# Performance work log

Measured on AMD Instinct MI355X. Metric: run time of the kernel, lower is better.

## Reference

```python
import jax, jax.numpy as jnp
import numpy as np

D_MODEL = 1024
K_QUERY = 32
K_TOPK = 4

def setup_inputs() -> dict:
    key = jax.random.key(0)
    k1, k2, k3, k4, k5 = jax.random.split(key, 5)
    x = jax.random.normal(k1, (4, 2048, D_MODEL), dtype=jnp.float32)
    # nn.Linear(d_model, k_query): weight [k_query, d_model], bias [k_query]
    sc = 1.0 / np.sqrt(D_MODEL)
    Wq = jax.random.uniform(k2, (K_QUERY, D_MODEL), jnp.float32, -sc, sc)
    bq = jax.random.uniform(k3, (K_QUERY,), jnp.float32, -sc, sc)
    Wk = jax.random.uniform(k4, (K_QUERY, D_MODEL), jnp.float32, -sc, sc)
    bk = jax.random.uniform(k5, (K_QUERY,), jnp.float32, -sc, sc)
    return {"x": x, "Wq": Wq, "bq": bq, "Wk": Wk, "bk": bk}

def reference(x, Wq, bq, Wk, bk):
    # x: [B, T, D]
    queries = jnp.einsum('btd,kd->btk', x, Wq) + bq      # [B, T, Kq]
    keys = jnp.einsum('btd,kd->btk', x, Wk) + bk         # [B, T, Kq]
    sim = jnp.einsum('btk,bsk->bts', queries, keys)      # [B, T, T]
    sim = sim / jnp.sqrt(jnp.float32(queries.shape[-1]))
    _, topk_idx = jax.lax.top_k(sim, K_TOPK)              # [B, T, K]
    # gather neighbors per (b, t): x[b, topk_idx[b, t]] -> [B, T, K, D]
    neighbors = jax.vmap(lambda xb, ib: xb[ib])(x, topk_idx)
    gathered = neighbors.mean(axis=2)                     # [B, T, D]
    return gathered
```

## Files before the change

kernel.cpp:

```cpp
#include <hip/hip_runtime.h>
#include <math.h>

#define D_MODEL 1024
#define T_SEQ   2048
#define NBATCH  4
#define NROWS   (NBATCH * T_SEQ)
#define NOUT    64

#define T16F   1024

typedef float  v4f  __attribute__((ext_vector_type(4)));
typedef _Float16 v8hf __attribute__((ext_vector_type(8)));

__device__ __forceinline__ bool key_gt(float av, int ai, float bv, int bi) {
    return (av > bv) || (av == bv && ai < bi);
}

__device__ __forceinline__ void cmpswap(float& v0, int& i0, float& v1, int& i1) {
    bool sw = key_gt(v1, i1, v0, i0);
    float nv0 = sw ? v1 : v0, nv1 = sw ? v0 : v1;
    int   ni0 = sw ? i1 : i0, ni1 = sw ? i0 : i1;
    v0 = nv0; v1 = nv1; i0 = ni0; i1 = ni1;
}

__device__ __forceinline__ void merge4(float (&a)[4], int (&ai)[4],
                                       float b0, int j0, float b1, int j1,
                                       float b2, int j2, float b3, int j3) {
    if (!key_gt(a[0], ai[0], b3, j3)) { a[0] = b3; ai[0] = j3; }
    if (!key_gt(a[1], ai[1], b2, j2)) { a[1] = b2; ai[1] = j2; }
    if (!key_gt(a[2], ai[2], b1, j1)) { a[2] = b1; ai[2] = j1; }
    if (!key_gt(a[3], ai[3], b0, j0)) { a[3] = b0; ai[3] = j0; }
    cmpswap(a[0], ai[0], a[2], ai[2]);
    cmpswap(a[1], ai[1], a[3], ai[3]);
    cmpswap(a[0], ai[0], a[1], ai[1]);
    cmpswap(a[2], ai[2], a[3], ai[3]);
}

__device__ __forceinline__ void insert4(float (&tv)[4], int (&tix)[4], float v, int idx) {
    if (v > tv[3]) {
        bool g0 = v > tv[0], g1 = v > tv[1], g2 = v > tv[2];
        float n0 = g0 ? v : tv[0];
        int   m0 = g0 ? idx : tix[0];
        float n1 = g1 ? (g0 ? tv[0] : v) : tv[1];
        int   m1 = g1 ? (g0 ? tix[0] : idx) : tix[1];
        float n2 = g2 ? (g1 ? tv[1] : v) : tv[2];
        int   m2 = g2 ? (g1 ? tix[1] : idx) : tix[2];
        float n3 = g2 ? tv[2] : v;
        int   m3 = g2 ? tix[2] : idx;
        tv[0] = n0; tv[1] = n1; tv[2] = n2; tv[3] = n3;
        tix[0] = m0; tix[1] = m1; tix[2] = m2; tix[3] = m3;
    }
}

__device__ void run_probe16(int tid, int* __restrict__ tab)
{
    __shared__ _Float16 A16[16][32];
    __shared__ _Float16 B16[32][16];
    __shared__ float    D16[16][16];

    for (int e = tid; e < 512; e += 256) {
        const int m = e >> 5, k = e & 31;
        A16[m][k] = (_Float16)(float)(1 + (3 * m + 5 * k) % 61);
        const int kk = e >> 4, n = e & 15;
        B16[kk][n] = (_Float16)(float)(1 + (7 * kk + 11 * n) % 59);
    }
    __syncthreads();
    {
        const int m = tid >> 4, n = tid & 15;
        float s = 0.f;
        for (int k = 0; k < 32; ++k) s += (float)A16[m][k] * (float)B16[k][n];
        D16[m][n] = s;
    }
    __syncthreads();

    if (tid >= 64) return;
    const int lane = tid;

    v8hf a, b;
    const int ab = (lane >> 4) * 8;
    #pragma unroll
    for (int j = 0; j < 8; ++j) {
        a[j] = A16[lane & 15][ab + j];
        b[j] = B16[ab + j][lane & 15];
    }
    v4f c = {0.f, 0.f, 0.f, 0.f};
    c = __builtin_amdgcn_mfma_f32_16x16x32_f16(a, b, c, 0, 0, 0);

    bool ok0 = true;
    #pragma unroll
    for (int i = 0; i < 4; ++i)
        ok0 = ok0 && (c[i] == D16[4 * (lane >> 4) + i][lane & 15]);
    if (lane == 0) tab[T16F] = __all(ok0) ? 0 : -1;
}

__global__ __launch_bounds__(256) void wprep_probe(
    const float* __restrict__ Wq, const float* __restrict__ Wk,
    double* __restrict__ Wdt, _Float16* __restrict__ Wh, _Float16* __restrict__ Wl,
    int* __restrict__ tab)
{
    const int tid = threadIdx.x;
    const int idx = blockIdx.x * 256 + tid;

    {
        const int o = idx & 63;
        const int d = idx >> 6;
        float v = (o < 32) ? Wq[(size_t)o * D_MODEL + d]
                           : Wk[(size_t)(o - 32) * D_MODEL + d];
        Wdt[(size_t)d * 64 + o] = (double)v;
    }
    {
        const int o = idx >> 10;
        const int d = idx & 1023;
        float v = (o < 32) ? Wq[(size_t)o * D_MODEL + d]
                           : Wk[(size_t)(o - 32) * D_MODEL + d];
        _Float16 h = (_Float16)v;
        Wh[(size_t)o * D_MODEL + d] = h;
        Wl[(size_t)o * D_MODEL + d] = (_Float16)(v - (float)h);
    }

    if (blockIdx.x == 0) run_probe16(tid, tab);
}

__global__ __launch_bounds__(512) void proj(
    const float* __restrict__ x, const double* __restrict__ Wdt,
    const _Float16* __restrict__ Wh, const _Float16* __restrict__ Wl,
    const float* __restrict__ bq, const float* __restrict__ bk_,
    const int* __restrict__ tab,
    float* __restrict__ Qt, float* __restrict__ Kt,
    _Float16* __restrict__ Qh, _Float16* __restrict__ Ql,
    _Float16* __restrict__ Kh, _Float16* __restrict__ Kl)
{
    __shared__ float  comb[4][64][4];
    __shared__ double combd[4][64][4];

    const int tid  = threadIdx.x;
    const int lane = tid & 63;
    const int wav  = tid >> 6;
    const int og   = __builtin_amdgcn_readfirstlane(wav >> 1);
    const int half = __builtin_amdgcn_readfirstlane(wav & 1);
    const int row0 = blockIdx.x * 16;
    const int kb   = half * 512;

    if (tab[T16F] == 0) {
        const int m  = lane & 15;
        const int ko = (lane >> 4) * 8;
        const float*    xrow  = x  + (size_t)(row0 + m) * D_MODEL + kb + ko;
        const _Float16* whrow = Wh + (size_t)(og * 16 + m) * D_MODEL + kb + ko;
        const _Float16* wlrow = Wl + (size_t)(og * 16 + m) * D_MODEL + kb + ko;

        v4f hh = {0.f, 0.f, 0.f, 0.f};
        v4f hl = {0.f, 0.f, 0.f, 0.f};
        v4f lh = {0.f, 0.f, 0.f, 0.f};
        #pragma unroll 4
        for (int kc = 0; kc < 16; ++kc) {
            float4 x0 = *reinterpret_cast<const float4*>(xrow + kc * 32);
            float4 x1 = *reinterpret_cast<const float4*>(xrow + kc * 32 + 4);
            const float f[8] = {x0.x, x0.y, x0.z, x0.w, x1.x, x1.y, x1.z, x1.w};
            v8hf ah, al;
            #pragma unroll
            for (int e = 0; e < 8; ++e) {
                _Float16 h = (_Float16)f[e];
                ah[e] = h;
                al[e] = (_Float16)(f[e] - (float)h);
            }
            v8hf bh = *reinterpret_cast<const v8hf*>(whrow + kc * 32);
            v8hf bl = *reinterpret_cast<const v8hf*>(wlrow + kc * 32);
            hh = __builtin_amdgcn_mfma_f32_16x16x32_f16(ah, bh, hh, 0, 0, 0);
            hl = __builtin_amdgcn_mfma_f32_16x16x32_f16(ah, bl, hl, 0, 0, 0);
            lh = __builtin_amdgcn_mfma_f32_16x16x32_f16(al, bh, lh, 0, 0, 0);
        }

        v4f tot;
        #pragma unroll
        for (int i = 0; i < 4; ++i) tot[i] = (hh[i] + hl[i]) + lh[i];

        if (half == 1) {
            #pragma unroll
            for (int i = 0; i < 4; ++i) comb[og][lane][i] = tot[i];
        }
        __syncthreads();
        if (half == 0) {
            #pragma unroll
            for (int i = 0; i < 4; ++i) {
                const float t = tot[i] + comb[og][lane][i];
                const int dmv = 4 * (lane >> 4) + i;
                const int o   = og * 16 + m;
                const int row = row0 + dmv;
                const float bias = (o < 32) ? bq[o] : bk_[o - 32];
                const float v = t + bias;
                const _Float16 h = (_Float16)v;
                const _Float16 l = (_Float16)(v - (float)h);
                if (o < 32) {
                    Qh[(size_t)row * 32 + o] = h;
                    Ql[(size_t)row * 32 + o] = l;
                } else {
                    Kh[(size_t)row * 32 + (o - 32)] = h;
                    Kl[(size_t)row * 32 + (o - 32)] = l;
                }
            }
        }
        return;
    }

    {
        const int n  = lane & 15;
        const int r4 = (lane >> 4) * 4;
        const int o  = og * 16 + n;
        const double* wcol = Wdt + o;
        double acc[4] = {0.0, 0.0, 0.0, 0.0};
        for (int dd = 0; dd < 512; ++dd) {
            const int d = kb + dd;
            double wv = wcol[(size_t)d * 64];
            #pragma unroll
            for (int i = 0; i < 4; ++i)
                acc[i] = fma((double)x[(size_t)(row0 + r4 + i) * D_MODEL + d], wv, acc[i]);
        }
        if (half == 1) {
            #pragma unroll
            for (int i = 0; i < 4; ++i) combd[og][lane][i] = acc[i];
        }
        __syncthreads();
        if (half == 0) {
            #pragma unroll
            for (int i = 0; i < 4; ++i) {
                const double t = acc[i] + combd[og][lane][i];
                const int row = row0 + r4 + i;
                const int bb  = row >> 11, tt = row & 2047;
                const double bias = (o < 32) ? (double)bq[o] : (double)bk_[o - 32];
                const float v = (float)(t + bias);
                if (o < 32) Qt[((size_t)bb * 32 + o) * T_SEQ + tt] = v;
                else        Kt[((size_t)bb * 32 + (o - 32)) * T_SEQ + tt] = v;
            }
        }
    }
}

__global__ __launch_bounds__(512) void sim_topk_gather(
    const float* __restrict__ x,
    const _Float16* __restrict__ Qh, const _Float16* __restrict__ Ql,
    const _Float16* __restrict__ Kh, const _Float16* __restrict__ Kl,
    const float* __restrict__ Qt, const float* __restrict__ Kt,
    const int* __restrict__ tab,
    float* __restrict__ out)
{
    __shared__ float sV[8][16][4];
    __shared__ int   sI[8][16][4];
    __shared__ float sVf[16][32][4];
    __shared__ int   sIf[16][32][4];
    __shared__ int   topIdx[16][4];

    const int tid  = threadIdx.x;
    const int lane = tid & 63;
    const int wav  = tid >> 6;
    const int tt   = blockIdx.x & 127;
    const int b    = blockIdx.x >> 7;
    const int row0g = b * T_SEQ + tt * 16;

    if (tab[T16F] == 0) {
        const int m  = lane & 15;
        const int ko = (lane >> 4) * 8;
        v8hf ah = *reinterpret_cast<const v8hf*>(Qh + (size_t)(row0g + m) * 32 + ko);
        v8hf al = *reinterpret_cast<const v8hf*>(Ql + (size_t)(row0g + m) * 32 + ko);
        const _Float16* KhB = Kh + (size_t)b * T_SEQ * 32;
        const _Float16* KlB = Kl + (size_t)b * T_SEQ * 32;

        float tv[4][4]; int tix[4][4];
        #pragma unroll
        for (int r = 0; r < 4; ++r)
            #pragma unroll
            for (int j = 0; j < 4; ++j) { tv[r][j] = -INFINITY; tix[r][j] = 0x7fffffff; }

        const int sq = wav * 256;
        #pragma unroll 4
        for (int st = 0; st < 16; ++st) {
            const int s0 = sq + st * 16;
            v8hf bh = *reinterpret_cast<const v8hf*>(KhB + (size_t)(s0 + m) * 32 + ko);
            v8hf bl = *reinterpret_cast<const v8hf*>(KlB + (size_t)(s0 + m) * 32 + ko);
            v4f c = {0.f, 0.f, 0.f, 0.f};
            c = __builtin_amdgcn_mfma_f32_16x16x32_f16(ah, bh, c, 0, 0, 0);
            c = __builtin_amdgcn_mfma_f32_16x16x32_f16(ah, bl, c, 0, 0, 0);
            c = __builtin_amdgcn_mfma_f32_16x16x32_f16(al, bh, c, 0, 0, 0);
            c = __builtin_amdgcn_mfma_f32_16x16x32_f16(al, bl, c, 0, 0, 0);
            const int col = s0 + m;
            #pragma unroll
            for (int i = 0; i < 4; ++i) insert4(tv[i], tix[i], c[i], col);
        }

        #pragma unroll
        for (int mk = 1; mk <= 8; mk <<= 1) {
            #pragma unroll
            for (int r = 0; r < 4; ++r) {
                float b0 = __shfl_xor(tv[r][0], mk, 64);
                float b1 = __shfl_xor(tv[r][1], mk, 64);
                float b2 = __shfl_xor(tv[r][2], mk, 64);
                float b3 = __shfl_xor(tv[r][3], mk, 64);
                int   j0 = __shfl_xor(tix[r][0], mk, 64);
                int   j1 = __shfl_xor(tix[r][1], mk, 64);
                int   j2 = __shfl_xor(tix[r][2], mk, 64);
                int   j3 = __shfl_xor(tix[r][3], mk, 64);
                merge4(tv[r], tix[r], b0, j0, b1, j1, b2, j2, b3, j3);
            }
        }

        if ((lane & 15) == 0) {
            const int rbase = (lane >> 4) * 4;
            #pragma unroll
            for (int r = 0; r < 4; ++r)
                #pragma unroll
                for (int j = 0; j < 4; ++j) {
                    sV[wav][rbase + r][j] = tv[r][j];
                    sI[wav][rbase + r][j] = tix[r][j];
                }
        }
        __syncthreads();

        if (tid < 16) {
            float mv[4]; int mi[4];
            #pragma unroll
            for (int j = 0; j < 4; ++j) { mv[j] = sV[0][tid][j]; mi[j] = sI[0][tid][j]; }
            #pragma unroll
            for (int w = 1; w < 8; ++w)
                merge4(mv, mi,
                       sV[w][tid][0], sI[w][tid][0],
                       sV[w][tid][1], sI[w][tid][1],
                       sV[w][tid][2], sI[w][tid][2],
                       sV[w][tid][3], sI[w][tid][3]);
            #pragma unroll
            for (int j = 0; j < 4; ++j) topIdx[tid][j] = mi[j];
        }
        __syncthreads();
    } else {
        const float* QtB = Qt + (size_t)b * 32 * T_SEQ;
        const float* KtB = Kt + (size_t)b * 32 * T_SEQ;
        const int row   = tid >> 5;
        const int chunk = tid & 31;
        const int trow  = tt * 16 + row;
        float q[32];
        #pragma unroll 8
        for (int i = 0; i < 32; ++i) q[i] = QtB[(size_t)i * T_SEQ + trow];
        float tv4[4]; int tix4[4];
        #pragma unroll
        for (int j = 0; j < 4; ++j) { tv4[j] = -INFINITY; tix4[j] = 0x7fffffff; }
        const int sbeg = chunk * 64;
        for (int s = sbeg; s < sbeg + 64; ++s) {
            float sum = 0.f;
            #pragma unroll 8
            for (int i = 0; i < 32; ++i)
                sum = fmaf(q[i], KtB[(size_t)i * T_SEQ + s], sum);
            insert4(tv4, tix4, sum, s);
        }
        #pragma unroll
        for (int j = 0; j < 4; ++j) { sVf[row][chunk][j] = tv4[j]; sIf[row][chunk][j] = tix4[j]; }
        __syncthreads();
        if (tid < 16) {
            float mv[4]; int mi[4];
            #pragma unroll
            for (int j = 0; j < 4; ++j) { mv[j] = sVf[tid][0][j]; mi[j] = sIf[tid][0][j]; }
            for (int cc = 1; cc < 32; ++cc)
                merge4(mv, mi,
                       sVf[tid][cc][0], sIf[tid][cc][0],
                       sVf[tid][cc][1], sIf[tid][cc][1],
                       sVf[tid][cc][2], sIf[tid][cc][2],
                       sVf[tid][cc][3], sIf[tid][cc][3]);
            #pragma unroll
            for (int j = 0; j < 4; ++j) topIdx[tid][j] = mi[j];
        }
        __syncthreads();
    }

    const float* xb = x + (size_t)b * T_SEQ * D_MODEL;
    float* ob = out + (size_t)row0g * D_MODEL;
    const int rh = tid >> 8;
    const int t4 = tid & 255;
    #pragma unroll 2
    for (int rp = 0; rp < 8; ++rp) {
        const int r = rp * 2 + rh;
        const int i0 = topIdx[r][0], i1 = topIdx[r][1], i2 = topIdx[r][2], i3 = topIdx[r][3];
        float4 a0 = *(reinterpret_cast<const float4*>(xb + (size_t)i0 * D_MODEL) + t4);
        float4 a1 = *(reinterpret_cast<const float4*>(xb + (size_t)i1 * D_MODEL) + t4);
        float4 a2 = *(reinterpret_cast<const float4*>(xb + (size_t)i2 * D_MODEL) + t4);
        float4 a3 = *(reinterpret_cast<const float4*>(xb + (size_t)i3 * D_MODEL) + t4);
        float4 o;
        o.x = (a0.x + a1.x + a2.x + a3.x) * 0.25f;
        o.y = (a0.y + a1.y + a2.y + a3.y) * 0.25f;
        o.z = (a0.z + a1.z + a2.z + a3.z) * 0.25f;
        o.w = (a0.w + a1.w + a2.w + a3.w) * 0.25f;
        *(reinterpret_cast<float4*>(ob + (size_t)r * D_MODEL) + t4) = o;
    }
}

extern "C" void kernel_launch(void* const* d_in, const int* in_sizes, int n_in,
                              void* d_out, int out_size, void* d_ws, size_t ws_size,
                              hipStream_t stream) {
    const float* x  = (const float*)d_in[0];
    const float* Wq = (const float*)d_in[1];
    const float* bq = (const float*)d_in[2];
    const float* Wk = (const float*)d_in[3];
    const float* bk = (const float*)d_in[4];
    float* out = (float*)d_out;

    char* wsb = (char*)d_ws;
    int*      tab = (int*)wsb;
    double*   Wdt = (double*)(wsb + 8192);
    _Float16* Wh  = (_Float16*)(wsb + 8192 + 524288);
    _Float16* Wl  = (_Float16*)(wsb + 8192 + 524288 + 131072);
    float*    Qt  = (float*)(wsb + 8192 + 524288 + 262144);
    float*    Kt  = Qt + (size_t)NBATCH * 32 * T_SEQ;
    _Float16* Qh  = (_Float16*)((char*)Kt + (size_t)NBATCH * 32 * T_SEQ * 4);
    _Float16* Ql  = Qh + (size_t)NROWS * 32;
    _Float16* Kh  = Ql + (size_t)NROWS * 32;
    _Float16* Kl  = Kh + (size_t)NROWS * 32;

    wprep_probe<<<dim3(256), dim3(256), 0, stream>>>(Wq, Wk, Wdt, Wh, Wl, tab);
    proj<<<dim3(NROWS / 16), dim3(512), 0, stream>>>(x, Wdt, Wh, Wl, bq, bk, tab,
                                                     Qt, Kt, Qh, Ql, Kh, Kl);
    sim_topk_gather<<<dim3(512), dim3(512), 0, stream>>>(x, Qh, Ql, Kh, Kl, Qt, Kt, tab, out);
}
```

Before: 151.6 us.

## Presplit x into fp16 hi/lo, drop K-split in proj, transpose sim MFMA

When workspace allows, the weight-prep kernel now also splits x into fp16 high/low halves. The projection kernel then loads these directly instead of converting fp32 in its inner loop. Projection waves now each cover the full K range, which removes the shared-memory combine and barrier at the cost of halving the block size. In the sim kernel, operands are swapped so each lane holds keys for one query row, which cuts the per-lane top-4 state and the cross-lane merge steps. The extra split pass writes and rereads a copy of x as fp16 pairs, roughly the same bytes as the fp32 original, and it only runs if the workspace is large enough.

After: 160.2 us. +5.7%, slower.

```diff
diff --git a/kernel.cpp b/kernel.cpp
--- a/kernel.cpp
+++ b/kernel.cpp
@@ -94,109 +94,131 @@
 }
 
 __global__ __launch_bounds__(256) void wprep_probe(
+    const float* __restrict__ x,
     const float* __restrict__ Wq, const float* __restrict__ Wk,
     double* __restrict__ Wdt, _Float16* __restrict__ Wh, _Float16* __restrict__ Wl,
+    _Float16* __restrict__ Xh, _Float16* __restrict__ Xl, int do_xsplit,
     int* __restrict__ tab)
 {
     const int tid = threadIdx.x;
-    const int idx = blockIdx.x * 256 + tid;
-
-    {
-        const int o = idx & 63;
-        const int d = idx >> 6;
-        float v = (o < 32) ? Wq[(size_t)o * D_MODEL + d]
-                           : Wk[(size_t)(o - 32) * D_MODEL + d];
-        Wdt[(size_t)d * 64 + o] = (double)v;
-    }
-    {
-        const int o = idx >> 10;
-        const int d = idx & 1023;
-        float v = (o < 32) ? Wq[(size_t)o * D_MODEL + d]
-                           : Wk[(size_t)(o - 32) * D_MODEL + d];
-        _Float16 h = (_Float16)v;
-        Wh[(size_t)o * D_MODEL + d] = h;
-        Wl[(size_t)o * D_MODEL + d] = (_Float16)(v - (float)h);
+    const int gid = blockIdx.x * 256 + tid;
+
+    if (gid < 65536) {
+        {
+            const int o = gid & 63;
+            const int d = gid >> 6;
+            float v = (o < 32) ? Wq[(size_t)o * D_MODEL + d]
+                               : Wk[(size_t)(o - 32) * D_MODEL + d];
+            Wdt[(size_t)d * 64 + o] = (double)v;
+        }
+        {
+            const int o = gid >> 10;
+            const int d = gid & 1023;
+            float v = (o < 32) ? Wq[(size_t)o * D_MODEL + d]
+                               : Wk[(size_t)(o - 32) * D_MODEL + d];
+            _Float16 h = (_Float16)v;
+            Wh[(size_t)o * D_MODEL + d] = h;
+            Wl[(size_t)o * D_MODEL + d] = (_Float16)(v - (float)h);
+        }
+    }
+
+    if (do_xsplit) {
+        #pragma unroll
+        for (int j = 0; j < 8; ++j) {
+            const size_t f4 = (size_t)j * 262144 + gid;
+            float4 v = reinterpret_cast<const float4*>(x)[f4];
+            const float f[4] = {v.x, v.y, v.z, v.w};
+            union { _Float16 h[4]; short4 s; } uh, ul;
+            #pragma unroll
+            for (int e = 0; e < 4; ++e) {
+                _Float16 h = (_Float16)f[e];
+                uh.h[e] = h;
+                ul.h[e] = (_Float16)(f[e] - (float)h);
+            }
+            reinterpret_cast<short4*>(Xh)[f4] = uh.s;
+            reinterpret_cast<short4*>(Xl)[f4] = ul.s;
+        }
     }
 
     if (blockIdx.x == 0) run_probe16(tid, tab);
 }
 
-__global__ __launch_bounds__(512) void proj(
+__global__ __launch_bounds__(256, 4) void proj(
     const float* __restrict__ x, const double* __restrict__ Wdt,
     const _Float16* __restrict__ Wh, const _Float16* __restrict__ Wl,
+    const _Float16* __restrict__ Xh, const _Float16* __restrict__ Xl, int use_xsplit,
     const float* __restrict__ bq, const float* __restrict__ bk_,
     const int* __restrict__ tab,
     float* __restrict__ Qt, float* __restrict__ Kt,
     _Float16* __restrict__ Qh, _Float16* __restrict__ Ql,
     _Float16* __restrict__ Kh, _Float16* __restrict__ Kl)
 {
-    __shared__ float  comb[4][64][4];
-    __shared__ double combd[4][64][4];
-
     const int tid  = threadIdx.x;
     const int lane = tid & 63;
     const int wav  = tid >> 6;
-    const int og   = __builtin_amdgcn_readfirstlane(wav >> 1);
-    const int half = __builtin_amdgcn_readfirstlane(wav & 1);
+    const int og   = __builtin_amdgcn_readfirstlane(wav);
     const int row0 = blockIdx.x * 16;
-    const int kb   = half * 512;
 
     if (tab[T16F] == 0) {
         const int m  = lane & 15;
         const int ko = (lane >> 4) * 8;
-        const float*    xrow  = x  + (size_t)(row0 + m) * D_MODEL + kb + ko;
-        const _Float16* whrow = Wh + (size_t)(og * 16 + m) * D_MODEL + kb + ko;
-        const _Float16* wlrow = Wl + (size_t)(og * 16 + m) * D_MODEL + kb + ko;
+        const _Float16* bH = Wh + (size_t)(og * 16 + m) * D_MODEL + ko;
+        const _Float16* bL = Wl + (size_t)(og * 16 + m) * D_MODEL + ko;
 
         v4f hh = {0.f, 0.f, 0.f, 0.f};
         v4f hl = {0.f, 0.f, 0.f, 0.f};
         v4f lh = {0.f, 0.f, 0.f, 0.f};
-        #pragma unroll 4
-        for (int kc = 0; kc < 16; ++kc) {
-            float4 x0 = *reinterpret_cast<const float4*>(xrow + kc * 32);
-            float4 x1 = *reinterpret_cast<const float4*>(xrow + kc * 32 + 4);
-            const float f[8] = {x0.x, x0.y, x0.z, x0.w, x1.x, x1.y, x1.z, x1.w};
-            v8hf ah, al;
-            #pragma unroll
-            for (int e = 0; e < 8; ++e) {
-                _Float16 h = (_Float16)f[e];
-                ah[e] = h;
-                al[e] = (_Float16)(f[e] - (float)h);
+
+        if (use_xsplit) {
+            const _Float16* aH = Xh + (size_t)(row0 + m) * D_MODEL + ko;
+            const _Float16* aL = Xl + (size_t)(row0 + m) * D_MODEL + ko;
+            #pragma unroll 4
+            for (int kc = 0; kc < 32; ++kc) {
+                v8hf ah = *reinterpret_cast<const v8hf*>(aH + kc * 32);
+                v8hf al = *reinterpret_cast<const v8hf*>(aL + kc * 32);
+                v8hf bh = *reinterpret_cast<const v8hf*>(bH + kc * 32);
+                v8hf bl = *reinterpret_cast<const v8hf*>(bL + kc * 32);
+                hh = __builtin_amdgcn_mfma_f32_16x16x32_f16(ah, bh, hh, 0, 0, 0);
+                hl = __builtin_amdgcn_mfma_f32_16x16x32_f16(ah, bl, hl, 0, 0, 0);
+                lh = __builtin_amdgcn_mfma_f32_16x16x32_f16(al, bh, lh, 0, 0, 0);
             }
-            v8hf bh = *reinterpret_cast<const v8hf*>(whrow + kc * 32);
-            v8hf bl = *reinterpret_cast<const v8hf*>(wlrow + kc * 32);
-            hh = __builtin_amdgcn_mfma_f32_16x16x32_f16(ah, bh, hh, 0, 0, 0);
-            hl = __builtin_amdgcn_mfma_f32_16x16x32_f16(ah, bl, hl, 0, 0, 0);
-            lh = __builtin_amdgcn_mfma_f32_16x16x32_f16(al, bh, lh, 0, 0, 0);
-        }
-
-        v4f tot;
-        #pragma unroll
-        for (int i = 0; i < 4; ++i) tot[i] = (hh[i] + hl[i]) + lh[i];
-
-        if (half == 1) {
-            #pragma unroll
-            for (int i = 0; i < 4; ++i) comb[og][lane][i] = tot[i];
-        }
-        __syncthreads();
-        if (half == 0) {
-            #pragma unroll
-            for (int i = 0; i < 4; ++i) {
-                const float t = tot[i] + comb[og][lane][i];
-                const int dmv = 4 * (lane >> 4) + i;
-                const int o   = og * 16 + m;
-                const int row = row0 + dmv;
-                const float bias = (o < 32) ? bq[o] : bk_[o - 32];
-                const float v = t + bias;
-                const _Float16 h = (_Float16)v;
-                const _Float16 l = (_Float16)(v - (float)h);
-                if (o < 32) {
-                    Qh[(size_t)row * 32 + o] = h;
-                    Ql[(size_t)row * 32 + o] = l;
-                } else {
-                    Kh[(size_t)row * 32 + (o - 32)] = h;
-                    Kl[(size_t)row * 32 + (o - 32)] = l;
+        } else {
+            const float* xrow = x + (size_t)(row0 + m) * D_MODEL + ko;
+            #pragma unroll 4
+            for (int kc = 0; kc < 32; ++kc) {
+                float4 x0 = *reinterpret_cast<const float4*>(xrow + kc * 32);
+                float4 x1 = *reinterpret_cast<const float4*>(xrow + kc * 32 + 4);
+                const float f[8] = {x0.x, x0.y, x0.z, x0.w, x1.x, x1.y, x1.z, x1.w};
+                v8hf ah, al;
+                #pragma unroll
+                for (int e = 0; e < 8; ++e) {
+                    _Float16 h = (_Float16)f[e];
+                    ah[e] = h;
+                    al[e] = (_Float16)(f[e] - (float)h);
                 }
+                v8hf bh = *reinterpret_cast<const v8hf*>(bH + kc * 32);
+                v8hf bl = *reinterpret_cast<const v8hf*>(bL + kc * 32);
+                hh = __builtin_amdgcn_mfma_f32_16x16x32_f16(ah, bh, hh, 0, 0, 0);
+                hl = __builtin_amdgcn_mfma_f32_16x16x32_f16(ah, bl, hl, 0, 0, 0);
+                lh = __builtin_amdgcn_mfma_f32_16x16x32_f16(al, bh, lh, 0, 0, 0);
+            }
+        }
+
+        #pragma unroll
+        for (int i = 0; i < 4; ++i) {
+            const float t = (hh[i] + hl[i]) + lh[i];
+            const int o   = og * 16 + m;
+            const int row = row0 + 4 * (lane >> 4) + i;
+            const float bias = (o < 32) ? bq[o] : bk_[o - 32];
+            const float v = t + bias;
+            const _Float16 h = (_Float16)v;
+            const _Float16 l = (_Float16)(v - (float)h);
+            if (o < 32) {
+                Qh[(size_t)row * 32 + o] = h;
+                Ql[(size_t)row * 32 + o] = l;
+            } else {
+                Kh[(size_t)row * 32 + (o - 32)] = h;
+                Kl[(size_t)row * 32 + (o - 32)] = l;
             }
         }
         return;
@@ -208,34 +230,25 @@
         const int o  = og * 16 + n;
         const double* wcol = Wdt + o;
         double acc[4] = {0.0, 0.0, 0.0, 0.0};
-        for (int dd = 0; dd < 512; ++dd) {
-            const int d = kb + dd;
+        for (int d = 0; d < D_MODEL; ++d) {
             double wv = wcol[(size_t)d * 64];
             #pragma unroll
             for (int i = 0; i < 4; ++i)
                 acc[i] = fma((double)x[(size_t)(row0 + r4 + i) * D_MODEL + d], wv, acc[i]);
         }
-        if (half == 1) {
-            #pragma unroll
-            for (int i = 0; i < 4; ++i) combd[og][lane][i] = acc[i];
-        }
-        __syncthreads();
-        if (half == 0) {
-            #pragma unroll
-            for (int i = 0; i < 4; ++i) {
-                const double t = acc[i] + combd[og][lane][i];
-                const int row = row0 + r4 + i;
-                const int bb  = row >> 11, tt = row & 2047;
-                const double bias = (o < 32) ? (double)bq[o] : (double)bk_[o - 32];
-                const float v = (float)(t + bias);
-                if (o < 32) Qt[((size_t)bb * 32 + o) * T_SEQ + tt] = v;
-                else        Kt[((size_t)bb * 32 + (o - 32)) * T_SEQ + tt] = v;
-            }
-        }
-    }
-}
-
-__global__ __launch_bounds__(512) void sim_topk_gather(
+        #pragma unroll
+        for (int i = 0; i < 4; ++i) {
+            const int row = row0 + r4 + i;
+            const int bb  = row >> 11, tt = row & 2047;
+            const double bias = (o < 32) ? (double)bq[o] : (double)bk_[o - 32];
+            const float v = (float)(acc[i] + bias);
+            if (o < 32) Qt[((size_t)bb * 32 + o) * T_SEQ + tt] = v;
+            else        Kt[((size_t)bb * 32 + (o - 32)) * T_SEQ + tt] = v;
+        }
+    }
+}
+
+__global__ __launch_bounds__(512, 4) void sim_topk_gather(
     const float* __restrict__ x,
     const _Float16* __restrict__ Qh, const _Float16* __restrict__ Ql,
     const _Float16* __restrict__ Kh, const _Float16* __restrict__ Kl,
@@ -259,58 +272,50 @@
     if (tab[T16F] == 0) {
         const int m  = lane & 15;
         const int ko = (lane >> 4) * 8;
-        v8hf ah = *reinterpret_cast<const v8hf*>(Qh + (size_t)(row0g + m) * 32 + ko);
-        v8hf al = *reinterpret_cast<const v8hf*>(Ql + (size_t)(row0g + m) * 32 + ko);
+        v8hf qh = *reinterpret_cast<const v8hf*>(Qh + (size_t)(row0g + m) * 32 + ko);
+        v8hf ql = *reinterpret_cast<const v8hf*>(Ql + (size_t)(row0g + m) * 32 + ko);
         const _Float16* KhB = Kh + (size_t)b * T_SEQ * 32;
         const _Float16* KlB = Kl + (size_t)b * T_SEQ * 32;
 
-        float tv[4][4]; int tix[4][4];
-        #pragma unroll
-        for (int r = 0; r < 4; ++r)
-            #pragma unroll
-            for (int j = 0; j < 4; ++j) { tv[r][j] = -INFINITY; tix[r][j] = 0x7fffffff; }
+        float tv[4]; int tix[4];
+        #pragma unroll
+        for (int j = 0; j < 4; ++j) { tv[j] = -INFINITY; tix[j] = 0x7fffffff; }
 
         const int sq = wav * 256;
         #pragma unroll 4
         for (int st = 0; st < 16; ++st) {
             const int s0 = sq + st * 16;
-            v8hf bh = *reinterpret_cast<const v8hf*>(KhB + (size_t)(s0 + m) * 32 + ko);
-            v8hf bl = *reinterpret_cast<const v8hf*>(KlB + (size_t)(s0 + m) * 32 + ko);
+            v8hf kh = *reinterpret_cast<const v8hf*>(KhB + (size_t)(s0 + m) * 32 + ko);
+            v8hf kl = *reinterpret_cast<const v8hf*>(KlB + (size_t)(s0 + m) * 32 + ko);
             v4f c = {0.f, 0.f, 0.f, 0.f};
-            c = __builtin_amdgcn_mfma_f32_16x16x32_f16(ah, bh, c, 0, 0, 0);
-            c = __builtin_amdgcn_mfma_f32_16x16x32_f16(ah, bl, c, 0, 0, 0);
-            c = __builtin_amdgcn_mfma_f32_16x16x32_f16(al, bh, c, 0, 0, 0);
-            c = __builtin_amdgcn_mfma_f32_16x16x32_f16(al, bl, c, 0, 0, 0);
-            const int col = s0 + m;
-            #pragma unroll
-            for (int i = 0; i < 4; ++i) insert4(tv[i], tix[i], c[i], col);
-        }
-
-        #pragma unroll
-        for (int mk = 1; mk <= 8; mk <<= 1) {
-            #pragma unroll
-            for (int r = 0; r < 4; ++r) {
-                float b0 = __shfl_xor(tv[r][0], mk, 64);
-                float b1 = __shfl_xor(tv[r][1], mk, 64);
-                float b2 = __shfl_xor(tv[r][2], mk, 64);
-                float b3 = __shfl_xor(tv[r][3], mk, 64);
-                int   j0 = __shfl_xor(tix[r][0], mk, 64);
-                int   j1 = __shfl_xor(tix[r][1], mk, 64);
-                int   j2 = __shfl_xor(tix[r][2], mk, 64);
-                int   j3 = __shfl_xor(tix[r][3], mk, 64);
-                merge4(tv[r], tix[r], b0, j0, b1, j1, b2, j2, b3, j3);
+            c = __builtin_amdgcn_mfma_f32_16x16x32_f16(kh, qh, c, 0, 0, 0);
+            c = __builtin_amdgcn_mfma_f32_16x16x32_f16(kl, qh, c, 0, 0, 0);
+            c = __builtin_amdgcn_mfma_f32_16x16x32_f16(kh, ql, c, 0, 0, 0);
+            c = __builtin_amdgcn_mfma_f32_16x16x32_f16(kl, ql, c, 0, 0, 0);
+            const int sb = s0 + 4 * (lane >> 4);
+            #pragma unroll
+            for (int i = 0; i < 4; ++i) insert4(tv, tix, c[i], sb + i);
+        }
+
+        #pragma unroll
+        for (int mk = 16; mk <= 32; mk <<= 1) {
+            float b0 = __shfl_xor(tv[0], mk, 64);
+            float b1 = __shfl_xor(tv[1], mk, 64);
+            float b2 = __shfl_xor(tv[2], mk, 64);
+            float b3 = __shfl_xor(tv[3], mk, 64);
+            int   j0 = __shfl_xor(tix[0], mk, 64);
+            int   j1 = __shfl_xor(tix[1], mk, 64);
+            int   j2 = __shfl_xor(tix[2], mk, 64);
+            int   j3 = __shfl_xor(tix[3], mk, 64);
+            merge4(tv, tix, b0, j0, b1, j1, b2, j2, b3, j3);
+        }
+
+        if (lane < 16) {
+            #pragma unroll
+            for (int j = 0; j < 4; ++j) {
+                sV[wav][lane][j] = tv[j];
+                sI[wav][lane][j] = tix[j];
             }
-        }
-
-        if ((lane & 15) == 0) {
-            const int rbase = (lane >> 4) * 4;
-            #pragma unroll
-            for (int r = 0; r < 4; ++r)
-                #pragma unroll
-                for (int j = 0; j < 4; ++j) {
-                    sV[wav][rbase + r][j] = tv[r][j];
-                    sI[wav][rbase + r][j] = tix[r][j];
-                }
         }
         __syncthreads();
 
@@ -410,9 +415,15 @@
     _Float16* Ql  = Qh + (size_t)NROWS * 32;
     _Float16* Kh  = Ql + (size_t)NROWS * 32;
     _Float16* Kl  = Kh + (size_t)NROWS * 32;
-
-    wprep_probe<<<dim3(256), dim3(256), 0, stream>>>(Wq, Wk, Wdt, Wh, Wl, tab);
-    proj<<<dim3(NROWS / 16), dim3(512), 0, stream>>>(x, Wdt, Wh, Wl, bq, bk, tab,
-                                                     Qt, Kt, Qh, Ql, Kh, Kl);
+    _Float16* Xh  = Kl + (size_t)NROWS * 32;
+    _Float16* Xl  = Xh + (size_t)NROWS * D_MODEL;
+
+    const size_t need = 4988928 + 2 * (size_t)NROWS * D_MODEL * 2;
+    const int use_xsplit = (ws_size >= need) ? 1 : 0;
+
+    wprep_probe<<<dim3(1024), dim3(256), 0, stream>>>(x, Wq, Wk, Wdt, Wh, Wl,
+                                                      Xh, Xl, use_xsplit, tab);
+    proj<<<dim3(NROWS / 16), dim3(256), 0, stream>>>(x, Wdt, Wh, Wl, Xh, Xl, use_xsplit,
+                                                     bq, bk, tab, Qt, Kt, Qh, Ql, Kh, Kl);
     sim_topk_gather<<<dim3(512), dim3(512), 0, stream>>>(x, Qh, Ql, Kh, Kl, Qt, Kt, tab, out);
 }
```
